# Kernel optimization log

Measured on AMD Instinct MI355X. Metric: run time of the kernel, lower is better.

## Reference

```python
import jax, jax.numpy as jnp
import numpy as np
from jax import lax

H = 256      # hidden_size
B = 256      # batch
S = 672      # encoder history length (7 days of 15-min steps)
T = 96       # target_length (hardcoded TARGET_LENGTH)
IN = 1       # input_size


def _lstm_cell(x, h, c, Wih, Whh, b):
    # PyTorch gate order: i, f, g, o. b = b_ih + b_hh (combined).
    gates = x @ Wih.T + h @ Whh.T + b            # [B, 4H]
    i, f, g, o = jnp.split(gates, 4, axis=-1)
    c = jax.nn.sigmoid(f) * c + jax.nn.sigmoid(i) * jnp.tanh(g)
    h = jax.nn.sigmoid(o) * jnp.tanh(c)
    return h, c


def _run_lstm_layer(xs, Wih, Whh, b):
    # xs: [S, B, in] -> outputs [S, B, H], final (h, c)
    bsz = xs.shape[1]
    h0 = jnp.zeros((bsz, Whh.shape[1]), xs.dtype)
    c0 = jnp.zeros_like(h0)

    def step(carry, x):
        h, c = _lstm_cell(x, carry[0], carry[1], Wih, Whh, b)
        return (h, c), h

    (h, c), ys = lax.scan(step, (h0, c0), xs)
    return ys, h, c


def setup_inputs() -> dict:
    key = jax.random.key(0)
    ks = jax.random.split(key, 18)
    kscale = 1.0 / np.sqrt(H)

    def u(k, shape):
        return jax.random.uniform(k, shape, jnp.float32, -kscale, kscale)

    inp = {
        "features": jax.random.normal(ks[0], (B, S, IN), jnp.float32),
        # encoder LSTM (2 layers)
        "enc_Wih0": u(ks[1], (4 * H, IN)),
        "enc_Whh0": u(ks[2], (4 * H, H)),
        "enc_b0":   u(ks[3], (4 * H,)),
        "enc_Wih1": u(ks[4], (4 * H, H)),
        "enc_Whh1": u(ks[5], (4 * H, H)),
        "enc_b1":   u(ks[6], (4 * H,)),
        # decoder LSTM (2 layers, input size 1)
        "dec_Wih0": u(ks[7], (4 * H, 1)),
        "dec_Whh0": u(ks[8], (4 * H, H)),
        "dec_b0":   u(ks[9], (4 * H,)),
        "dec_Wih1": u(ks[10], (4 * H, H)),
        "dec_Whh1": u(ks[11], (4 * H, H)),
        "dec_b1":   u(ks[12], (4 * H,)),
        # output head: Linear(H,H) -> ReLU -> (Dropout=id at eval) -> Linear(H,1)
        "out_W1": u(ks[13], (H, H)),
        "out_b1": u(ks[14], (H,)),
        "out_W2": u(ks[15], (1, H)),
        "out_b2": u(ks[16], (1,)),
    }
    return inp


def reference(features, enc_Wih0, enc_Whh0, enc_b0, enc_Wih1, enc_Whh1, enc_b1,
              dec_Wih0, dec_Whh0, dec_b0, dec_Wih1, dec_Whh1, dec_b1,
              out_W1, out_b1, out_W2, out_b2):
    # --- encoder: 2-layer LSTM over the history ---
    xs = jnp.swapaxes(features, 0, 1)                       # [S, B, 1]
    ys0, eh0, ec0 = _run_lstm_layer(xs, enc_Wih0, enc_Whh0, enc_b0)
    _,   eh1, ec1 = _run_lstm_layer(ys0, enc_Wih1, enc_Whh1, enc_b1)

    x0 = jnp.zeros((features.shape[0], 1), features.dtype)  # [B, 1]

    def dec_step(carry, _):
        x, h0, c0, h1, c1 = carry
        h0, c0 = _lstm_cell(x, h0, c0, dec_Wih0, dec_Whh0, dec_b0)
        h1, c1 = _lstm_cell(h0, h1, c1, dec_Wih1, dec_Whh1, dec_b1)
        hid = jnp.maximum(h1 @ out_W1.T + out_b1, 0.0)      # ReLU (Dropout=id)
        pred = hid @ out_W2.T + out_b2                      # [B, 1]
        return (pred, h0, c0, h1, c1), pred[:, 0]

    _, preds = lax.scan(dec_step, (x0, eh0, ec0, eh1, ec1), None, length=T)
    return preds.T                                          # [B, T]
```

## Files before the change

kernel.cpp:

```cpp
#include <hip/hip_runtime.h>


#define S_LEN 672
#define T_LEN 96
#define HDIM  256
#define SPIN_MAX (1 << 14)

typedef short short8 __attribute__((ext_vector_type(8)));
typedef float f32x4  __attribute__((ext_vector_type(4)));
typedef unsigned short u16;

#define OFF_FLAG 0
#define OFF_FE   1024
#define OFF_FD   (OFF_FE + 16*16*32)
#define OFF_PART (OFF_FD + 16*16*32)
#define ZERO_END (OFF_PART + 2*16*256*4)
#define OFF_H0   ZERO_END
#define OFF_H1   (OFF_H0 + 16*2*4096*2)
#define OFF_F0   (OFF_H1 + 16*2*4096*2)
#define OFF_F1   (OFF_F0 + 16*4096*2)
#define OFF_C0   (OFF_F1 + 16*4096*2)
#define OFF_C1   (OFF_C0 + 256*256*4)

__device__ __forceinline__ unsigned short f2bf(float f) {
  unsigned u = __float_as_uint(f);
  u += 0x7FFFu + ((u >> 16) & 1u);
  return (unsigned short)(u >> 16);
}
__device__ __forceinline__ float bf2f(unsigned short s) {
  return __uint_as_float(((unsigned)s) << 16);
}
__device__ __forceinline__ float ld_scalar(const void* p, long idx, int mode) {
  if (mode) return bf2f(((const u16*)p)[idx]);
  return ((const float*)p)[idx];
}
__device__ __forceinline__ short8 ld_frag8(const void* p, long row, long ld, long k0, int mode) {
  if (mode) {
    return *(const short8*)((const u16*)p + row * ld + k0);
  } else {
    const float* f = (const float*)p + row * ld + k0;
    short8 r;
#pragma unroll
    for (int i = 0; i < 8; i++) r[i] = (short)f2bf(f[i]);
    return r;
  }
}
__device__ __forceinline__ void st_out(void* out, size_t idx, float v, int mode) {
  if (mode) ((u16*)out)[idx] = f2bf(v);
  else      ((float*)out)[idx] = v;
}
__device__ __forceinline__ float sigm(float x) { return 1.f / (1.f + __expf(-x)); }

__device__ __forceinline__ f32x4 mfma_bf16(short8 a, short8 b, f32x4 c) {
  return __builtin_amdgcn_mfma_f32_16x16x32_bf16(a, b, c, 0, 0, 0);
}

__device__ __forceinline__ void ld32B(const u16* b, short8* c0, short8* c1) {
  asm volatile(
    "global_load_dwordx4 %0, %2, off sc0 sc1\n\t"
    "global_load_dwordx4 %1, %2, off offset:16 sc0 sc1"
    : "=&v"(*c0), "=&v"(*c1) : "v"(b) : "memory");
}
__device__ __forceinline__ void issue2(const u16* base, short8* t) {
  asm volatile(
    "global_load_dwordx4 %0, %2, off sc0 sc1\n\t"
    "global_load_dwordx4 %1, %2, off offset:64 sc0 sc1"
    : "=&v"(t[0]), "=&v"(t[1]) : "v"(base) : "memory");
}
__device__ __forceinline__ void st16(u16* p, unsigned short v) {
  asm volatile("global_store_short %0, %1, off sc0 sc1"
               :: "v"(p), "v"((unsigned)v) : "memory");
}
__device__ __forceinline__ void stf32(float* p, float v) {
  asm volatile("global_store_dword %0, %1, off sc0 sc1" :: "v"(p), "v"(v) : "memory");
}
__device__ __forceinline__ float ldf32(const float* p) {
  float v;
  asm volatile("global_load_dword %0, %1, off sc0 sc1\n\ts_waitcnt vmcnt(0)"
               : "=&v"(v) : "v"(p) : "memory");
  __builtin_amdgcn_sched_barrier(0);
  return v;
}
__device__ __forceinline__ void waitv0() {
  asm volatile("s_waitcnt vmcnt(0)" ::: "memory");
  __builtin_amdgcn_sched_barrier(0);
}

__device__ __forceinline__ void wg_publish(unsigned* fa, unsigned e) {
  asm volatile("s_waitcnt vmcnt(0)" ::: "memory");
  __syncthreads();
  if (threadIdx.x == 0)
    asm volatile("global_store_dword %0, %1, off sc0 sc1" :: "v"(fa), "v"(e) : "memory");
}
__device__ __forceinline__ void pollge(const unsigned* flags, unsigned E) {
  const unsigned* addr = flags + (threadIdx.x & 15) * 8;
  int spin = 0;
  for (;;) {
    unsigned v;
    asm volatile("global_load_dword %0, %1, off sc0 sc1\n\ts_waitcnt vmcnt(0)"
                 : "=&v"(v) : "v"(addr) : "memory");
    if (__all(v >= E)) break;
    if (++spin > SPIN_MAX) break;
    __builtin_amdgcn_s_sleep(1);
  }
  __builtin_amdgcn_sched_barrier(0);
}

__global__ void detect_mode(const unsigned* __restrict__ feat, unsigned* __restrict__ flag) {
  const int t = threadIdx.x;
  int cnt = 0;
#pragma unroll
  for (int i = 0; i < 8; i++) {
    const unsigned wv = feat[t * 8 + i];
    const unsigned e = (wv >> 7) & 0xFFu;
    cnt += (e >= 100u && e <= 130u) ? 1 : 0;
  }
#pragma unroll
  for (int o = 32; o > 0; o >>= 1) cnt += __shfl_down(cnt, o, 64);
  if (t == 0) flag[0] = (cnt >= 256) ? 1u : 0u;
}

__global__ void __launch_bounds__(256, 1)
enc_kernel(const void* __restrict__ feat,
           const void* __restrict__ Wih0, const void* __restrict__ Whh0, const void* __restrict__ b0,
           const void* __restrict__ Wih1, const void* __restrict__ Whh1, const void* __restrict__ b1,
           char* __restrict__ ws) {
  const int mode = (int)*(const unsigned*)(ws + OFF_FLAG);
  const int tid  = threadIdx.x;
  const int lane = tid & 63;
  const int w    = tid >> 6;
  const int bId  = blockIdx.x;
  const int g    = (bId & 7) * 2 + ((bId >> 3) & 1);
  const int m    = bId >> 4;

  const int fcol = lane & 15;
  const int kq   = lane >> 4;
  const int chq  = m * 16 + w * 4 + kq;
  const int bgl  = g * 16 + fcol;
  const int sr   = tid >> 4;
  const int sc2  = (tid & 15) * 2;

  unsigned* fe_g = (unsigned*)(ws + OFF_FE) + g * 128;
  u16* h0s = (u16*)(ws + OFF_H0) + (size_t)g * 2 * 4096;
  u16* h1s = (u16*)(ws + OFF_H1) + (size_t)g * 2 * 4096;
  u16* f0s = (u16*)(ws + OFF_F0) + (size_t)g * 4096;
  u16* f1s = (u16*)(ws + OFF_F1) + (size_t)g * 4096;
  float* c0ws = (float*)(ws + OFF_C0);
  float* c1ws = (float*)(ws + OFF_C1);

  __shared__ short8 sh0[16][33];
  __shared__ short8 sh1[16][33];

  const int n    = 16 * w + fcol;
  const int grow = (n & 3) * HDIM + m * 16 + (n >> 2);
  short8 wh0[8], wi1[8], wh1[8];
#pragma unroll
  for (int kf = 0; kf < 8; kf++) {
    const int k0 = kf * 32 + kq * 8;
    wh0[kf] = ld_frag8(Whh0, grow, HDIM, k0, mode);
    wi1[kf] = ld_frag8(Wih1, grow, HDIM, k0, mode);
    wh1[kf] = ld_frag8(Whh1, grow, HDIM, k0, mode);
  }
  float wx[4], bb0[4], bb1[4];
#pragma unroll
  for (int gt = 0; gt < 4; gt++) {
    wx[gt]  = ld_scalar(Wih0, gt * HDIM + chq, mode);
    bb0[gt] = ld_scalar(b0,   gt * HDIM + chq, mode);
    bb1[gt] = ld_scalar(b1,   gt * HDIM + chq, mode);
  }
  float c0 = 0.f, c1 = 0.f, h0keep = 0.f, h1fin = 0.f;

  for (int t = 0; t <= S_LEN; t++) {
    const int pr = (t + 1) & 1, pw = t & 1;
    short8 a0[8], a1[8];
    if (t >= 1) {
      pollge(fe_g, (unsigned)t);
      short8 va0, va1, vb0, vb1;
      ld32B(h0s + pr * 4096 + tid * 16, &va0, &va1);
      if (t >= 2) ld32B(h1s + pr * 4096 + tid * 16, &vb0, &vb1);
      waitv0();
      sh0[sr][sc2] = va0; sh0[sr][sc2 + 1] = va1;
      if (t >= 2) { sh1[sr][sc2] = vb0; sh1[sr][sc2 + 1] = vb1; }
      __syncthreads();
#pragma unroll
      for (int kf = 0; kf < 8; kf++) a0[kf] = sh0[fcol][kf * 4 + kq];
      if (t >= 2) {
#pragma unroll
        for (int kf = 0; kf < 8; kf++) a1[kf] = sh1[fcol][kf * 4 + kq];
      }
    }

    f32x4 acc0 = {0.f, 0.f, 0.f, 0.f}, acc1 = {0.f, 0.f, 0.f, 0.f};
    if (t >= 1 && t < S_LEN) {
#pragma unroll
      for (int kf = 0; kf < 8; kf++) acc0 = mfma_bf16(wh0[kf], a0[kf], acc0);
    }
    if (t >= 1) {
#pragma unroll
      for (int kf = 0; kf < 8; kf++) acc1 = mfma_bf16(wi1[kf], a0[kf], acc1);
      if (t >= 2) {
#pragma unroll
        for (int kf = 0; kf < 8; kf++) acc1 = mfma_bf16(wh1[kf], a1[kf], acc1);
      }
    }
    if (t < S_LEN) {
      const float x = ld_scalar(feat, (long)bgl * S_LEN + t, mode);
      const float gi = acc0[0] + x * wx[0] + bb0[0];
      const float gf = acc0[1] + x * wx[1] + bb0[1];
      const float gg = acc0[2] + x * wx[2] + bb0[2];
      const float go = acc0[3] + x * wx[3] + bb0[3];
      c0 = sigm(gf) * c0 + sigm(gi) * tanhf(gg);
      const float h0v = sigm(go) * tanhf(c0);
      h0keep = h0v;
      st16(h0s + pw * 4096 + fcol * 256 + chq, f2bf(h0v));
    }
    if (t >= 1) {
      const float gi = acc1[0] + bb1[0];
      const float gf = acc1[1] + bb1[1];
      const float gg = acc1[2] + bb1[2];
      const float go = acc1[3] + bb1[3];
      c1 = sigm(gf) * c1 + sigm(gi) * tanhf(gg);
      const float h1v = sigm(go) * tanhf(c1);
      if (t < S_LEN) st16(h1s + pw * 4096 + fcol * 256 + chq, f2bf(h1v));
      else h1fin = h1v;
    }
    wg_publish(fe_g + m * 8, (unsigned)(t + 1));
  }
  f0s[fcol * 256 + chq] = f2bf(h0keep);
  f1s[fcol * 256 + chq] = f2bf(h1fin);
  c0ws[(size_t)bgl * HDIM + chq] = c0;
  c1ws[(size_t)bgl * HDIM + chq] = c1;
}

__global__ void __launch_bounds__(256, 1)
dec_kernel(const void* __restrict__ Wih0, const void* __restrict__ Whh0, const void* __restrict__ b0,
           const void* __restrict__ Wih1, const void* __restrict__ Whh1, const void* __restrict__ b1,
           const void* __restrict__ W1, const void* __restrict__ b1h, const void* __restrict__ W2,
           const void* __restrict__ b2, char* __restrict__ ws, void* __restrict__ out) {
  const int mode = (int)*(const unsigned*)(ws + OFF_FLAG);
  const int tid  = threadIdx.x;
  const int lane = tid & 63;
  const int w    = tid >> 6;
  const int bId  = blockIdx.x;
  const int g    = (bId & 7) * 2 + ((bId >> 3) & 1);
  const int m    = bId >> 4;

  const int fcol = lane & 15;
  const int kq   = lane >> 4;
  const int chq  = m * 16 + w * 4 + kq;
  const int bgl  = g * 16 + fcol;
  const int sr   = tid >> 4;
  const int sc2  = (tid & 15) * 2;

  unsigned* fd_g = (unsigned*)(ws + OFF_FD) + g * 128;
  u16* h0s = (u16*)(ws + OFF_H0) + (size_t)g * 2 * 4096;
  u16* h1s = (u16*)(ws + OFF_H1) + (size_t)g * 2 * 4096;
  u16* f0s = (u16*)(ws + OFF_F0) + (size_t)g * 4096;
  u16* f1s = (u16*)(ws + OFF_F1) + (size_t)g * 4096;
  float* partial = (float*)(ws + OFF_PART);
  float* c0ws = (float*)(ws + OFF_C0);
  float* c1ws = (float*)(ws + OFF_C1);

  __shared__ short8 sh0[16][33];
  __shared__ short8 sh1[16][33];
  __shared__ float part[4 * 256];
  __shared__ float redv[256];
  __shared__ float xacc[256];

  const int n    = 16 * w + fcol;
  const int grow = (n & 3) * HDIM + m * 16 + (n >> 2);
  short8 wh0[8], wi1[8], wh1[8], ww1[2];
#pragma unroll
  for (int kf = 0; kf < 8; kf++) {
    const int k0 = kf * 32 + kq * 8;
    wh0[kf] = ld_frag8(Whh0, grow, HDIM, k0, mode);
    wi1[kf] = ld_frag8(Wih1, grow, HDIM, k0, mode);
    wh1[kf] = ld_frag8(Whh1, grow, HDIM, k0, mode);
  }
#pragma unroll
  for (int kf2 = 0; kf2 < 2; kf2++) {
    const int k0 = w * 64 + kf2 * 32 + kq * 8;
    ww1[kf2] = ld_frag8(W1, m * 16 + fcol, HDIM, k0, mode);
  }
  float wx[4], bb0[4], bb1[4];
#pragma unroll
  for (int gt = 0; gt < 4; gt++) {
    wx[gt]  = ld_scalar(Wih0, gt * HDIM + chq, mode);
    bb0[gt] = ld_scalar(b0,   gt * HDIM + chq, mode);
    bb1[gt] = ld_scalar(b1,   gt * HDIM + chq, mode);
  }
  const int hb = tid & 15, hcl = tid >> 4;
  const float b1hv = ld_scalar(b1h, m * 16 + hcl, mode);
  const float w2v  = ld_scalar(W2,  m * 16 + hcl, mode);
  const float b2v  = ld_scalar(b2, 0, mode);

  float c0 = c0ws[(size_t)bgl * HDIM + chq];
  float c1 = c1ws[(size_t)bgl * HDIM + chq];

  for (int s = 0; s < T_LEN; s++) {
    const int ppr = (s - 1) & 1, pcur = s & 1;
    float x = 0.f;
    {
      if (s > 0) pollge(fd_g, (unsigned)(3 * s));
      short8 va0, va1;
      float pv = 0.f;
      if (s > 0) {
        ld32B(h0s + ppr * 4096 + tid * 16, &va0, &va1);
        pv = ldf32(partial + (((size_t)ppr * 16 + g) * 16 + (tid >> 4)) * 16 + (tid & 15));
      } else {
        ld32B(f0s + tid * 16, &va0, &va1);
        waitv0();
      }
      sh0[sr][sc2] = va0; sh0[sr][sc2 + 1] = va1;
      if (s > 0) xacc[(tid & 15) * 16 + (tid >> 4)] = pv;
      __syncthreads();
      if (s > 0) {
#pragma unroll
        for (int j = 0; j < 16; j++) x += xacc[fcol * 16 + j];
        if (m == 0 && tid < 16)
          st_out(out, (size_t)(g * 16 + tid) * T_LEN + (s - 1), x, mode);
      }
      short8 a0[8];
#pragma unroll
      for (int kf = 0; kf < 8; kf++) a0[kf] = sh0[fcol][kf * 4 + kq];
      f32x4 acc = {0.f, 0.f, 0.f, 0.f};
#pragma unroll
      for (int kf = 0; kf < 8; kf++) acc = mfma_bf16(wh0[kf], a0[kf], acc);
      const float gi = acc[0] + x * wx[0] + bb0[0];
      const float gf = acc[1] + x * wx[1] + bb0[1];
      const float gg = acc[2] + x * wx[2] + bb0[2];
      const float go = acc[3] + x * wx[3] + bb0[3];
      c0 = sigm(gf) * c0 + sigm(gi) * tanhf(gg);
      const float h0v = sigm(go) * tanhf(c0);
      st16(h0s + pcur * 4096 + fcol * 256 + chq, f2bf(h0v));
      wg_publish(fd_g + m * 8, (unsigned)(3 * s + 1));
    }
    {
      pollge(fd_g, (unsigned)(3 * s + 1));
      short8 va0, va1, vb0, vb1;
      ld32B(h0s + pcur * 4096 + tid * 16, &va0, &va1);
      ld32B(((s == 0) ? f1s : (h1s + ppr * 4096)) + tid * 16, &vb0, &vb1);
      waitv0();
      sh0[sr][sc2] = va0; sh0[sr][sc2 + 1] = va1;
      sh1[sr][sc2] = vb0; sh1[sr][sc2 + 1] = vb1;
      __syncthreads();
      short8 ay[8], a1[8];
#pragma unroll
      for (int kf = 0; kf < 8; kf++) {
        ay[kf] = sh0[fcol][kf * 4 + kq];
        a1[kf] = sh1[fcol][kf * 4 + kq];
      }
      f32x4 acc = {0.f, 0.f, 0.f, 0.f};
#pragma unroll
      for (int kf = 0; kf < 8; kf++) {
        acc = mfma_bf16(wi1[kf], ay[kf], acc);
        acc = mfma_bf16(wh1[kf], a1[kf], acc);
      }
      const float gi = acc[0] + bb1[0];
      const float gf = acc[1] + bb1[1];
      const float gg = acc[2] + bb1[2];
      const float go = acc[3] + bb1[3];
      c1 = sigm(gf) * c1 + sigm(gi) * tanhf(gg);
      const float h1v = sigm(go) * tanhf(c1);
      st16(h1s + pcur * 4096 + fcol * 256 + chq, f2bf(h1v));
      wg_publish(fd_g + m * 8, (unsigned)(3 * s + 2));
    }
    {
      pollge(fd_g, (unsigned)(3 * s + 2));
      short8 ah[2];
      issue2(h1s + pcur * 4096 + fcol * 256 + w * 64 + kq * 8, ah);
      waitv0();
      f32x4 acc = {0.f, 0.f, 0.f, 0.f};
      acc = mfma_bf16(ww1[0], ah[0], acc);
      acc = mfma_bf16(ww1[1], ah[1], acc);
      *(f32x4*)&part[w * 256 + fcol * 16 + kq * 4] = acc;
      __syncthreads();
      float hid = part[0 * 256 + hb * 16 + hcl] + part[1 * 256 + hb * 16 + hcl]
                + part[2 * 256 + hb * 16 + hcl] + part[3 * 256 + hb * 16 + hcl] + b1hv;
      hid = fmaxf(hid, 0.f);
      redv[hcl * 16 + hb] = hid * w2v;
      __syncthreads();
      if (tid < 16) {
        float a = (m == 0) ? b2v : 0.f;
#pragma unroll
        for (int cc = 0; cc < 16; cc++) a += redv[cc * 16 + tid];
        stf32(partial + (((size_t)pcur * 16 + g) * 16 + m) * 16 + tid, a);
      }
      wg_publish(fd_g + m * 8, (unsigned)(3 * s + 3));
    }
  }
  if (m == 0) {
    pollge(fd_g, (unsigned)(3 * T_LEN));
    const float pv = ldf32(partial + (((size_t)1 * 16 + g) * 16 + (tid >> 4)) * 16 + (tid & 15));
    xacc[(tid & 15) * 16 + (tid >> 4)] = pv;
    __syncthreads();
    if (tid < 16) {
      float x = 0.f;
#pragma unroll
      for (int j = 0; j < 16; j++) x += xacc[tid * 16 + j];
      st_out(out, (size_t)(g * 16 + tid) * T_LEN + (T_LEN - 1), x, mode);
    }
  }
}

extern "C" void kernel_launch(void* const* d_in, const int* in_sizes, int n_in,
                              void* d_out, int out_size, void* d_ws, size_t ws_size,
                              hipStream_t stream) {
  char* ws = (char*)d_ws;
  hipMemsetAsync(ws, 0, ZERO_END, stream);
  detect_mode<<<1, 64, 0, stream>>>((const unsigned*)d_in[0], (unsigned*)(ws + OFF_FLAG));
  enc_kernel<<<256, 256, 0, stream>>>(d_in[0], d_in[1], d_in[2], d_in[3],
                                      d_in[4], d_in[5], d_in[6], ws);
  dec_kernel<<<256, 256, 0, stream>>>(d_in[7], d_in[8], d_in[9], d_in[10], d_in[11], d_in[12],
                                      d_in[13], d_in[14], d_in[15], d_in[16], ws, d_out);
}
```

Before: 3.199 ms.

## Split encoder step flags per layer with per-wave publishing to overlap layers

Replaces the single per-workgroup step flag with two flag arrays, one per encoder layer, written by each wave's lane 0 rather than through a workgroup-wide publish. The layer-0 flag is published right after h0 is stored, before the layer-1 recurrent MFMAs, so other workgroups can start the next layer-0 step sooner. The layer-1 flag is published lazily at the start of the next step. The polling loop now checks both flags across 64 lanes, and the feature load moves ahead of the poll to hide its latency. This adds more polling traffic and a subtler cross-layer ordering protocol.

```diff
diff --git a/kernel.cpp b/kernel.cpp
--- a/kernel.cpp
+++ b/kernel.cpp
@@ -11,8 +11,9 @@
 typedef unsigned short u16;
 
 #define OFF_FLAG 0
-#define OFF_FE   1024
-#define OFF_FD   (OFF_FE + 16*16*32)
+#define OFF_FE0  1024
+#define OFF_FE1  (OFF_FE0 + 4096)
+#define OFF_FD   (OFF_FE1 + 4096)
 #define OFF_PART (OFF_FD + 16*16*32)
 #define ZERO_END (OFF_PART + 2*16*256*4)
 #define OFF_H0   ZERO_END
@@ -70,6 +71,9 @@
 __device__ __forceinline__ void st16(u16* p, unsigned short v) {
   asm volatile("global_store_short %0, %1, off sc0 sc1"
                :: "v"(p), "v"((unsigned)v) : "memory");
+}
+__device__ __forceinline__ void st32(unsigned* p, unsigned v) {
+  asm volatile("global_store_dword %0, %1, off sc0 sc1" :: "v"(p), "v"(v) : "memory");
 }
 __device__ __forceinline__ void stf32(float* p, float v) {
   asm volatile("global_store_dword %0, %1, off sc0 sc1" :: "v"(p), "v"(v) : "memory");
@@ -140,7 +144,8 @@
   const int sr   = tid >> 4;
   const int sc2  = (tid & 15) * 2;
 
-  unsigned* fe_g = (unsigned*)(ws + OFF_FE) + g * 128;
+  unsigned* fe0g = (unsigned*)(ws + OFF_FE0) + g * 64;
+  unsigned* fe1g = (unsigned*)(ws + OFF_FE1) + g * 64;
   u16* h0s = (u16*)(ws + OFF_H0) + (size_t)g * 2 * 4096;
   u16* h1s = (u16*)(ws + OFF_H1) + (size_t)g * 2 * 4096;
   u16* f0s = (u16*)(ws + OFF_F0) + (size_t)g * 4096;
@@ -173,8 +178,35 @@
   for (int t = 0; t <= S_LEN; t++) {
     const int pr = (t + 1) & 1, pw = t & 1;
     short8 a0[8], a1[8];
+    float x = 0.f;
     if (t >= 1) {
-      pollge(fe_g, (unsigned)t);
+      asm volatile("s_waitcnt vmcnt(0)" ::: "memory");
+      __builtin_amdgcn_sched_barrier(0);
+      if (t >= 2 && lane == 0) st32(fe1g + m * 4 + w, (unsigned)(t - 1));
+      if (t < S_LEN) x = ld_scalar(feat, (long)bgl * S_LEN + t, mode);
+      const unsigned* f0a = fe0g + lane;
+      const unsigned* f1a = fe1g + lane;
+      int spin = 0;
+      if (t >= 2) {
+        for (;;) {
+          unsigned v0, v1;
+          asm volatile("global_load_dword %0, %2, off sc0 sc1\n\t"
+                       "global_load_dword %1, %3, off sc0 sc1\n\t"
+                       "s_waitcnt vmcnt(0)"
+                       : "=&v"(v0), "=&v"(v1) : "v"(f0a), "v"(f1a) : "memory");
+          if (__all((v0 >= (unsigned)t) && (v1 >= (unsigned)(t - 1)))) break;
+          if (++spin > SPIN_MAX) break;
+        }
+      } else {
+        for (;;) {
+          unsigned v0;
+          asm volatile("global_load_dword %0, %1, off sc0 sc1\n\ts_waitcnt vmcnt(0)"
+                       : "=&v"(v0) : "v"(f0a) : "memory");
+          if (__all(v0 >= (unsigned)t)) break;
+          if (++spin > SPIN_MAX) break;
+        }
+      }
+      __builtin_amdgcn_sched_barrier(0);
       short8 va0, va1, vb0, vb1;
       ld32B(h0s + pr * 4096 + tid * 16, &va0, &va1);
       if (t >= 2) ld32B(h1s + pr * 4096 + tid * 16, &vb0, &vb1);
@@ -188,6 +220,8 @@
 #pragma unroll
         for (int kf = 0; kf < 8; kf++) a1[kf] = sh1[fcol][kf * 4 + kq];
       }
+    } else {
+      x = ld_scalar(feat, (long)bgl * S_LEN + t, mode);
     }
 
     f32x4 acc0 = {0.f, 0.f, 0.f, 0.f}, acc1 = {0.f, 0.f, 0.f, 0.f};
@@ -195,16 +229,7 @@
 #pragma unroll
       for (int kf = 0; kf < 8; kf++) acc0 = mfma_bf16(wh0[kf], a0[kf], acc0);
     }
-    if (t >= 1) {
-#pragma unroll
-      for (int kf = 0; kf < 8; kf++) acc1 = mfma_bf16(wi1[kf], a0[kf], acc1);
-      if (t >= 2) {
-#pragma unroll
-        for (int kf = 0; kf < 8; kf++) acc1 = mfma_bf16(wh1[kf], a1[kf], acc1);
-      }
-    }
     if (t < S_LEN) {
-      const float x = ld_scalar(feat, (long)bgl * S_LEN + t, mode);
       const float gi = acc0[0] + x * wx[0] + bb0[0];
       const float gf = acc0[1] + x * wx[1] + bb0[1];
       const float gg = acc0[2] + x * wx[2] + bb0[2];
@@ -215,6 +240,19 @@
       st16(h0s + pw * 4096 + fcol * 256 + chq, f2bf(h0v));
     }
     if (t >= 1) {
+#pragma unroll
+      for (int kf = 0; kf < 8; kf++) acc1 = mfma_bf16(wi1[kf], a0[kf], acc1);
+    }
+    if (t < S_LEN) {
+      asm volatile("s_waitcnt vmcnt(0)" ::: "memory");
+      __builtin_amdgcn_sched_barrier(0);
+      if (lane == 0) st32(fe0g + m * 4 + w, (unsigned)(t + 1));
+    }
+    if (t >= 1) {
+      if (t >= 2) {
+#pragma unroll
+        for (int kf = 0; kf < 8; kf++) acc1 = mfma_bf16(wh1[kf], a1[kf], acc1);
+      }
       const float gi = acc1[0] + bb1[0];
       const float gf = acc1[1] + bb1[1];
       const float gg = acc1[2] + bb1[2];
@@ -224,7 +262,6 @@
       if (t < S_LEN) st16(h1s + pw * 4096 + fcol * 256 + chq, f2bf(h1v));
       else h1fin = h1v;
     }
-    wg_publish(fe_g + m * 8, (unsigned)(t + 1));
   }
   f0s[fcol * 256 + chq] = f2bf(h0keep);
   f1s[fcol * 256 + chq] = f2bf(h1fin);
```

New measurement: 5.087 ms. +59.0%, slower.

## Use 512-thread encoder blocks so each batch group syncs across 8 blocks

Applied to the files above, without the earlier changes.

The encoder grid goes from 256 blocks of 256 threads to 128 blocks of 512 threads, so each block owns two 16-channel hidden slices. Each batch group now has 8 cooperating blocks instead of 16. The per-step flag poll therefore checks 8 flags, the flag region shrinks, and each thread loads 16 B of the shared hidden state instead of 32 B. The aim is to cut cross-block barrier latency on the 672-step serial recurrence. In exchange, each block does twice the work per step, and intra-block syncs now span 8 waves.

```diff
diff --git a/kernel.cpp b/kernel.cpp
--- a/kernel.cpp
+++ b/kernel.cpp
@@ -12,7 +12,7 @@
 
 #define OFF_FLAG 0
 #define OFF_FE   1024
-#define OFF_FD   (OFF_FE + 16*16*32)
+#define OFF_FD   (OFF_FE + 16*8*32)
 #define OFF_PART (OFF_FD + 16*16*32)
 #define ZERO_END (OFF_PART + 2*16*256*4)
 #define OFF_H0   ZERO_END
@@ -55,6 +55,10 @@
   return __builtin_amdgcn_mfma_f32_16x16x32_bf16(a, b, c, 0, 0, 0);
 }
 
+__device__ __forceinline__ void ld16B(const u16* b, short8* c0) {
+  asm volatile("global_load_dwordx4 %0, %1, off sc0 sc1"
+               : "=&v"(*c0) : "v"(b) : "memory");
+}
 __device__ __forceinline__ void ld32B(const u16* b, short8* c0, short8* c1) {
   asm volatile(
     "global_load_dwordx4 %0, %2, off sc0 sc1\n\t"
@@ -92,7 +96,20 @@
   if (threadIdx.x == 0)
     asm volatile("global_store_dword %0, %1, off sc0 sc1" :: "v"(fa), "v"(e) : "memory");
 }
-__device__ __forceinline__ void pollge(const unsigned* flags, unsigned E) {
+__device__ __forceinline__ void pollge8(const unsigned* flags, unsigned E) {
+  const unsigned* addr = flags + (threadIdx.x & 7) * 8;
+  int spin = 0;
+  for (;;) {
+    unsigned v;
+    asm volatile("global_load_dword %0, %1, off sc0 sc1\n\ts_waitcnt vmcnt(0)"
+                 : "=&v"(v) : "v"(addr) : "memory");
+    if (__all(v >= E)) break;
+    if (++spin > SPIN_MAX) break;
+    __builtin_amdgcn_s_sleep(1);
+  }
+  __builtin_amdgcn_sched_barrier(0);
+}
+__device__ __forceinline__ void pollge16(const unsigned* flags, unsigned E) {
   const unsigned* addr = flags + (threadIdx.x & 15) * 8;
   int spin = 0;
   for (;;) {
@@ -120,7 +137,7 @@
   if (t == 0) flag[0] = (cnt >= 256) ? 1u : 0u;
 }
 
-__global__ void __launch_bounds__(256, 1)
+__global__ void __launch_bounds__(512, 1)
 enc_kernel(const void* __restrict__ feat,
            const void* __restrict__ Wih0, const void* __restrict__ Whh0, const void* __restrict__ b0,
            const void* __restrict__ Wih1, const void* __restrict__ Whh1, const void* __restrict__ b1,
@@ -129,18 +146,20 @@
   const int tid  = threadIdx.x;
   const int lane = tid & 63;
   const int w    = tid >> 6;
+  const int wl   = w & 3;
   const int bId  = blockIdx.x;
   const int g    = (bId & 7) * 2 + ((bId >> 3) & 1);
   const int m    = bId >> 4;
+  const int sh   = m * 2 + (w >> 2);
 
   const int fcol = lane & 15;
   const int kq   = lane >> 4;
-  const int chq  = m * 16 + w * 4 + kq;
+  const int chq  = sh * 16 + wl * 4 + kq;
   const int bgl  = g * 16 + fcol;
-  const int sr   = tid >> 4;
-  const int sc2  = (tid & 15) * 2;
-
-  unsigned* fe_g = (unsigned*)(ws + OFF_FE) + g * 128;
+  const int sr   = tid >> 5;
+  const int scc  = tid & 31;
+
+  unsigned* fe_g = (unsigned*)(ws + OFF_FE) + g * 64;
   u16* h0s = (u16*)(ws + OFF_H0) + (size_t)g * 2 * 4096;
   u16* h1s = (u16*)(ws + OFF_H1) + (size_t)g * 2 * 4096;
   u16* f0s = (u16*)(ws + OFF_F0) + (size_t)g * 4096;
@@ -151,8 +170,8 @@
   __shared__ short8 sh0[16][33];
   __shared__ short8 sh1[16][33];
 
-  const int n    = 16 * w + fcol;
-  const int grow = (n & 3) * HDIM + m * 16 + (n >> 2);
+  const int n    = 16 * wl + fcol;
+  const int grow = (n & 3) * HDIM + sh * 16 + (n >> 2);
   short8 wh0[8], wi1[8], wh1[8];
 #pragma unroll
   for (int kf = 0; kf < 8; kf++) {
@@ -174,13 +193,13 @@
     const int pr = (t + 1) & 1, pw = t & 1;
     short8 a0[8], a1[8];
     if (t >= 1) {
-      pollge(fe_g, (unsigned)t);
-      short8 va0, va1, vb0, vb1;
-      ld32B(h0s + pr * 4096 + tid * 16, &va0, &va1);
-      if (t >= 2) ld32B(h1s + pr * 4096 + tid * 16, &vb0, &vb1);
+      pollge8(fe_g, (unsigned)t);
+      short8 va, vb;
+      ld16B(h0s + pr * 4096 + tid * 8, &va);
+      if (t >= 2) ld16B(h1s + pr * 4096 + tid * 8, &vb);
       waitv0();
-      sh0[sr][sc2] = va0; sh0[sr][sc2 + 1] = va1;
-      if (t >= 2) { sh1[sr][sc2] = vb0; sh1[sr][sc2 + 1] = vb1; }
+      sh0[sr][scc] = va;
+      if (t >= 2) sh1[sr][scc] = vb;
       __syncthreads();
 #pragma unroll
       for (int kf = 0; kf < 8; kf++) a0[kf] = sh0[fcol][kf * 4 + kq];
@@ -301,7 +320,7 @@
     const int ppr = (s - 1) & 1, pcur = s & 1;
     float x = 0.f;
     {
-      if (s > 0) pollge(fd_g, (unsigned)(3 * s));
+      if (s > 0) pollge16(fd_g, (unsigned)(3 * s));
       short8 va0, va1;
       float pv = 0.f;
       if (s > 0) {
@@ -336,7 +355,7 @@
       wg_publish(fd_g + m * 8, (unsigned)(3 * s + 1));
     }
     {
-      pollge(fd_g, (unsigned)(3 * s + 1));
+      pollge16(fd_g, (unsigned)(3 * s + 1));
       short8 va0, va1, vb0, vb1;
       ld32B(h0s + pcur * 4096 + tid * 16, &va0, &va1);
       ld32B(((s == 0) ? f1s : (h1s + ppr * 4096)) + tid * 16, &vb0, &vb1);
@@ -366,7 +385,7 @@
       wg_publish(fd_g + m * 8, (unsigned)(3 * s + 2));
     }
     {
-      pollge(fd_g, (unsigned)(3 * s + 2));
+      pollge16(fd_g, (unsigned)(3 * s + 2));
       short8 ah[2];
       issue2(h1s + pcur * 4096 + fcol * 256 + w * 64 + kq * 8, ah);
       waitv0();
@@ -390,7 +409,7 @@
     }
   }
   if (m == 0) {
-    pollge(fd_g, (unsigned)(3 * T_LEN));
+    pollge16(fd_g, (unsigned)(3 * T_LEN));
     const float pv = ldf32(partial + (((size_t)1 * 16 + g) * 16 + (tid >> 4)) * 16 + (tid & 15));
     xacc[(tid & 15) * 16 + (tid >> 4)] = pv;
     __syncthreads();
@@ -409,7 +428,7 @@
   char* ws = (char*)d_ws;
   hipMemsetAsync(ws, 0, ZERO_END, stream);
   detect_mode<<<1, 64, 0, stream>>>((const unsigned*)d_in[0], (unsigned*)(ws + OFF_FLAG));
-  enc_kernel<<<256, 256, 0, stream>>>(d_in[0], d_in[1], d_in[2], d_in[3],
+  enc_kernel<<<128, 512, 0, stream>>>(d_in[0], d_in[1], d_in[2], d_in[3],
                                       d_in[4], d_in[5], d_in[6], ws);
   dec_kernel<<<256, 256, 0, stream>>>(d_in[7], d_in[8], d_in[9], d_in[10], d_in[11], d_in[12],
                                       d_in[13], d_in[14], d_in[15], d_in[16], ws, d_out);
```

Result: faster. 2.756 ms (median of 2 runs) (-13.8%).
